# Performance work log

Hardware: AMD Instinct MI355X
Metric: run time of the kernel (lower is better)

## Reference

```python
import jax, jax.numpy as jnp
import numpy as np


def setup_inputs() -> dict:
    key = jax.random.key(0)
    ks = jax.random.split(key, 10)
    N, E, IN, H, OUT = 100000, 1250000, 64, 128, 64
    inp = {
        "x": jax.random.normal(ks[0], (N, IN), dtype=jnp.float32),
        "edge_index": jax.random.randint(ks[1], (2, E), 0, N, dtype=jnp.int64),
        "W1x": jax.random.normal(ks[2], (IN, H), dtype=jnp.float32) * 0.1,
        "b1x": jnp.zeros((H,), jnp.float32),
        "W2x": jax.random.normal(ks[3], (H, H), dtype=jnp.float32) * 0.1,
        "b2x": jnp.zeros((H,), jnp.float32),
        "W1a": jax.random.normal(ks[4], (IN, H), dtype=jnp.float32) * 0.1,
        "b1a": jnp.zeros((H,), jnp.float32),
        "W2a": jax.random.normal(ks[5], (H, H), dtype=jnp.float32) * 0.1,
        "b2a": jnp.zeros((H,), jnp.float32),
        "Wc": jax.random.normal(ks[6], (2 * H, H), dtype=jnp.float32) * 0.1,
        "bc": jnp.zeros((H,), jnp.float32),
        "Wcls": jax.random.normal(ks[7], (H, OUT), dtype=jnp.float32) * 0.1,
        "bcls": jnp.zeros((OUT,), jnp.float32),
        "num_nodes": N,
    }
    return inp


def _normalize_adj(edge_index, num_nodes):
    # add self loops, then D^{-1/2} A D^{-1/2} edge weights (deg counted on rows)
    loops = jnp.arange(num_nodes, dtype=edge_index.dtype)
    ei = jnp.concatenate([edge_index, jnp.stack([loops, loops])], axis=1)
    row, col = ei[0], ei[1]
    deg = jax.ops.segment_sum(jnp.ones(row.shape[0], jnp.float32), row,
                              num_segments=num_nodes)
    dinv = jnp.where(deg > 0, jax.lax.rsqrt(deg), 0.0)
    ew = dinv[row] * dinv[col]
    return row, col, ew


def reference(x, edge_index, W1x, b1x, W2x, b2x, W1a, b1a, W2a, b2a,
              Wc, bc, Wcls, bcls, num_nodes):
    row, col, ew = _normalize_adj(edge_index, num_nodes)
    # sparse adjacency aggregation: gather, scale, scatter-add
    agg = jax.ops.segment_sum(x[col] * ew[:, None], row, num_segments=num_nodes)
    # dual-branch MLPs
    h_x = jax.nn.relu(x @ W1x + b1x) @ W2x + b2x
    h_a = jax.nn.relu(agg @ W1a + b1a) @ W2a + b2a
    h = jnp.concatenate([h_x, h_a], axis=1) @ Wc + bc
    h = jax.nn.relu(h)  # dropout: eval mode (identity)
    return h @ Wcls + bcls
```

## Files before the change

### kernel.cpp

```cpp
#include <hip/hip_runtime.h>
#include <stdint.h>

typedef unsigned short u16;
typedef unsigned int u32;
typedef __attribute__((ext_vector_type(8))) short frag_ab;
typedef __attribute__((ext_vector_type(4))) float f32x4;

__device__ __forceinline__ u16 f2b(float f) {
  unsigned u = __float_as_uint(f);
  return (u16)((u + 0x7fffu + ((u >> 16) & 1u)) >> 16);
}
__device__ __forceinline__ float b2f(u16 u) {
  return __uint_as_float(((unsigned)u) << 16);
}

__device__ __forceinline__ int detect64(const int* __restrict__ ei32) {
  int v = ei32[2 * (threadIdx.x & 63) + 1];
  unsigned long long b = __ballot(v == 0);
  return (b == ~0ULL) ? 1 : 0;
}

__device__ __forceinline__ int edge_at(const void* ei, long pos, int is64) {
  if (is64) return (int)((const long long*)ei)[pos];
  return ((const int*)ei)[pos];
}

__global__ __launch_bounds__(256) void k_bhist_cvt(
    const void* __restrict__ ei, int E, int CH, int NB, int NBpad,
    int* __restrict__ bh,
    const float* __restrict__ x, u16* __restrict__ xb, long n64) {
  __shared__ int cnt[512];
  const int k = blockIdx.x, tid = threadIdx.x;
  const int is64 = detect64((const int*)ei);
  for (long i = ((long)k * 256 + tid) * 8; i < n64; i += 65536L * 8) {
    float4 v0 = *(const float4*)(x + i);
    float4 v1 = *(const float4*)(x + i + 4);
    frag_ab o;
    o[0] = (short)f2b(v0.x); o[1] = (short)f2b(v0.y);
    o[2] = (short)f2b(v0.z); o[3] = (short)f2b(v0.w);
    o[4] = (short)f2b(v1.x); o[5] = (short)f2b(v1.y);
    o[6] = (short)f2b(v1.z); o[7] = (short)f2b(v1.w);
    *(frag_ab*)(xb + i) = o;
  }
  for (int t = tid; t < NB; t += 256) cnt[t] = 0;
  __syncthreads();
  int e0 = k * CH, e1 = min(E, e0 + CH);
  for (int e = e0 + tid; e < e1; e += 256)
    atomicAdd(&cnt[edge_at(ei, e, is64) >> 9], 1);
  __syncthreads();
  for (int t = tid; t < NB; t += 256) bh[k * NBpad + t] = cnt[t];
}

__global__ __launch_bounds__(256) void k_cscan(
    int* __restrict__ bh, int* __restrict__ bstart, int NB, int NBpad, int E) {
  __shared__ int s[256];
  const int b = threadIdx.x;
  int tot = 0;
  if (b < NB)
    for (int k = 0; k < 256; ++k) tot += bh[k * NBpad + b];
  s[b] = (b < NB) ? tot : 0;
  __syncthreads();
  for (int off = 1; off < 256; off <<= 1) {
    int u = (b >= off) ? s[b - off] : 0;
    __syncthreads();
    s[b] += u;
    __syncthreads();
  }
  int excl = s[b] - tot;
  if (b < NB) {
    bstart[b] = excl;
    int run = excl;
    for (int k = 0; k < 256; ++k) {
      int t = bh[k * NBpad + b];
      bh[k * NBpad + b] = run;
      run += t;
    }
  }
  if (b == 0) bstart[NB] = E;
}

__global__ __launch_bounds__(256) void k_partition(
    const void* __restrict__ ei, int E, int CH, int NB, int NBpad,
    const int* __restrict__ bh, u32* __restrict__ staged) {
  __shared__ int cur[512];
  const int k = blockIdx.x, tid = threadIdx.x;
  const int is64 = detect64((const int*)ei);
  for (int t = tid; t < NB; t += 256) cur[t] = bh[k * NBpad + t];
  __syncthreads();
  int e0 = k * CH, e1 = min(E, e0 + CH);
  for (int e = e0 + tid; e < e1; e += 256) {
    int r = edge_at(ei, e, is64);
    int c = edge_at(ei, (long)E + e, is64);
    int pos = atomicAdd(&cur[r >> 9], 1);
    staged[pos] = ((u32)(r & 511) << 23) | (u32)c;
  }
}

__global__ __launch_bounds__(1024) void k_csr_bucket(
    const u32* __restrict__ staged, const int* __restrict__ bstart,
    int* __restrict__ rowptr, float* __restrict__ dinv,
    u32* __restrict__ cols, int N, int E) {
  __shared__ int cnt[512];
  __shared__ int cur[512];
  const int b = blockIdx.x, tid = threadIdx.x;
  const int r0 = b << 9;
  if (tid < 512) cnt[tid] = 0;
  __syncthreads();
  const int j0 = bstart[b], j1 = bstart[b + 1];
  for (int j = j0 + tid; j < j1; j += 1024)
    atomicAdd(&cnt[staged[j] >> 23], 1);
  __syncthreads();
  if (tid < 512) cur[tid] = cnt[tid];
  __syncthreads();
  for (int off = 1; off < 512; off <<= 1) {
    int v = 0;
    if (tid < 512 && tid >= off) v = cur[tid - off];
    __syncthreads();
    if (tid < 512) cur[tid] += v;
    __syncthreads();
  }
  int myStart = 0;
  if (tid < 512) {
    myStart = j0 + cur[tid] - cnt[tid];
    int r = r0 + tid;
    if (r < N) {
      rowptr[r] = myStart;
      dinv[r] = rsqrtf((float)cnt[tid] + 1.0f);
    }
  }
  __syncthreads();
  if (tid < 512) cur[tid] = myStart;
  if (b == 0 && tid == 0) rowptr[N] = E;
  __syncthreads();
  for (int j = j0 + tid; j < j1; j += 1024) {
    u32 v = staged[j];
    int rl = v >> 23;
    int pos = atomicAdd(&cur[rl], 1);
    cols[pos] = v & 0x7FFFFF;
  }
}

__global__ __launch_bounds__(256) void k_aggregate(
    const int* __restrict__ rowptr, const u32* __restrict__ cols,
    const u16* __restrict__ xb, const float* __restrict__ dinv,
    u16* __restrict__ aggb, int N) {
  int q = (blockIdx.x * 256 + threadIdx.x) >> 6;
  int f = threadIdx.x & 63;
  int r0 = q * 2, r1 = q * 2 + 1;
  if (r0 >= N) return;
  const bool has1 = (r1 < N);
  int j0 = rowptr[r0], e0 = rowptr[r0 + 1];
  int j1 = has1 ? rowptr[r1] : 0;
  int e1 = has1 ? rowptr[r1 + 1] : 0;
  float d0 = dinv[r0];
  float d1 = has1 ? dinv[r1] : 0.f;
  float acc0 = b2f(xb[(long)r0 * 64 + f]) * d0;
  float acc1 = has1 ? b2f(xb[(long)r1 * 64 + f]) * d1 : 0.f;
  while (j0 + 4 <= e0 && j1 + 4 <= e1) {
    int ca0 = cols[j0], ca1 = cols[j0 + 1], ca2 = cols[j0 + 2], ca3 = cols[j0 + 3];
    int cb0 = cols[j1], cb1 = cols[j1 + 1], cb2 = cols[j1 + 2], cb3 = cols[j1 + 3];
    float xa0 = b2f(xb[(long)ca0 * 64 + f]);
    float xa1 = b2f(xb[(long)ca1 * 64 + f]);
    float xa2 = b2f(xb[(long)ca2 * 64 + f]);
    float xa3 = b2f(xb[(long)ca3 * 64 + f]);
    float xb0 = b2f(xb[(long)cb0 * 64 + f]);
    float xb1 = b2f(xb[(long)cb1 * 64 + f]);
    float xb2 = b2f(xb[(long)cb2 * 64 + f]);
    float xb3 = b2f(xb[(long)cb3 * 64 + f]);
    float wa0 = dinv[ca0], wa1 = dinv[ca1], wa2 = dinv[ca2], wa3 = dinv[ca3];
    float wb0 = dinv[cb0], wb1 = dinv[cb1], wb2 = dinv[cb2], wb3 = dinv[cb3];
    acc0 = fmaf(xa0, wa0, acc0); acc1 = fmaf(xb0, wb0, acc1);
    acc0 = fmaf(xa1, wa1, acc0); acc1 = fmaf(xb1, wb1, acc1);
    acc0 = fmaf(xa2, wa2, acc0); acc1 = fmaf(xb2, wb2, acc1);
    acc0 = fmaf(xa3, wa3, acc0); acc1 = fmaf(xb3, wb3, acc1);
    j0 += 4; j1 += 4;
  }
  for (; j0 + 4 <= e0; j0 += 4) {
    int c0 = cols[j0], c1 = cols[j0 + 1], c2 = cols[j0 + 2], c3 = cols[j0 + 3];
    float x0 = b2f(xb[(long)c0 * 64 + f]);
    float x1 = b2f(xb[(long)c1 * 64 + f]);
    float x2 = b2f(xb[(long)c2 * 64 + f]);
    float x3 = b2f(xb[(long)c3 * 64 + f]);
    acc0 = fmaf(x0, dinv[c0], acc0);
    acc0 = fmaf(x1, dinv[c1], acc0);
    acc0 = fmaf(x2, dinv[c2], acc0);
    acc0 = fmaf(x3, dinv[c3], acc0);
  }
  for (; j0 < e0; ++j0) {
    int c = cols[j0];
    acc0 = fmaf(b2f(xb[(long)c * 64 + f]), dinv[c], acc0);
  }
  for (; j1 + 4 <= e1; j1 += 4) {
    int c0 = cols[j1], c1 = cols[j1 + 1], c2 = cols[j1 + 2], c3 = cols[j1 + 3];
    float x0 = b2f(xb[(long)c0 * 64 + f]);
    float x1 = b2f(xb[(long)c1 * 64 + f]);
    float x2 = b2f(xb[(long)c2 * 64 + f]);
    float x3 = b2f(xb[(long)c3 * 64 + f]);
    acc1 = fmaf(x0, dinv[c0], acc1);
    acc1 = fmaf(x1, dinv[c1], acc1);
    acc1 = fmaf(x2, dinv[c2], acc1);
    acc1 = fmaf(x3, dinv[c3], acc1);
  }
  for (; j1 < e1; ++j1) {
    int c = cols[j1];
    acc1 = fmaf(b2f(xb[(long)c * 64 + f]), dinv[c], acc1);
  }
  aggb[(long)r0 * 64 + f] = f2b(acc0 * d0);
  if (has1) aggb[(long)r1 * 64 + f] = f2b(acc1 * d1);
}

__global__ __launch_bounds__(256) void k_wpack(
    const float* __restrict__ W1x, const float* __restrict__ W1a,
    const float* __restrict__ W2x, const float* __restrict__ W2a,
    const float* __restrict__ Wc, const float* __restrict__ b2x,
    const float* __restrict__ b2a, const float* __restrict__ bc,
    const float* __restrict__ Wcls,
    u16* __restrict__ W1xf, u16* __restrict__ W1af,
    u16* __restrict__ Wxpf, u16* __restrict__ Wapf,
    u16* __restrict__ Wclsf, float* __restrict__ bp) {
  const int blk = blockIdx.x, t = threadIdx.x;
  if (blk < 128) {
    const bool isX = blk < 64;
    int i = (isX ? blk : blk - 64) * 256 + t;
    const float* W2 = isX ? W2x : W2a;
    const float* wc = isX ? Wc : Wc + 128 * 128;
    int b = i & 7, l = (i >> 3) & 63, fi = i >> 9;
    int kb = fi & 3, nb = fi >> 2;
    int k = kb * 32 + (l >> 4) * 8 + b;
    int n = nb * 16 + (l & 15);
    float s = 0.f;
    for (int m = 0; m < 128; ++m) s = fmaf(W2[k * 128 + m], wc[m * 128 + n], s);
    (isX ? Wxpf : Wapf)[i] = f2b(s);
  } else if (blk < 224) {
    const float* W; u16* dst; int K, Nc, i0;
    if (blk < 160)      { W = W1x;  dst = W1xf;  K = 64;  Nc = 128; i0 = blk - 128; }
    else if (blk < 192) { W = W1a;  dst = W1af;  K = 64;  Nc = 128; i0 = blk - 160; }
    else                { W = Wcls; dst = Wclsf; K = 128; Nc = 64;  i0 = blk - 192; }
    int i = i0 * 256 + t;
    if (i < K * Nc) {
      int b = i & 7, l = (i >> 3) & 63, fi = i >> 9;
      int KB = K >> 5;
      int kb = fi % KB, nb = fi / KB;
      int k = kb * 32 + (l >> 4) * 8 + b;
      int n = nb * 16 + (l & 15);
      dst[i] = f2b(W[k * Nc + n]);
    }
  } else if (t < 128) {
    float s = bc[t];
    for (int m = 0; m < 128; ++m)
      s += b2x[m] * Wc[m * 128 + t] + b2a[m] * Wc[(128 + m) * 128 + t];
    bp[t] = s;
  }
}

__global__ __launch_bounds__(256) void k_mlp(
    const u16* __restrict__ xb, const u16* __restrict__ aggb,
    const u16* __restrict__ W1xf, const u16* __restrict__ W1af,
    const float* __restrict__ b1x, const float* __restrict__ b1a,
    const u16* __restrict__ Wxpf, const u16* __restrict__ Wapf,
    const float* __restrict__ bp,
    const u16* __restrict__ Wclsf, const float* __restrict__ bcls,
    float* __restrict__ out, int N) {
  __shared__ u16 H1[64 * 256];
  __shared__ u16 H2[64 * 128];
  const int w = threadIdx.x >> 6;
  const int lane = threadIdx.x & 63;
  const int m0 = blockIdx.x * 64;
  const int lm = lane & 15;
  const int lq = lane >> 4;

  for (int br = 0; br < 2; ++br) {
    const u16* A = br ? aggb : xb;
    const u16* Wf = br ? W1af : W1xf;
    const float* bias = br ? b1a : b1x;
    frag_ab a[4][2];
#pragma unroll
    for (int rt = 0; rt < 4; ++rt) {
      const u16* ap = A + (long)(m0 + rt * 16 + lm) * 64 + lq * 8;
      a[rt][0] = *(const frag_ab*)(ap);
      a[rt][1] = *(const frag_ab*)(ap + 32);
    }
#pragma unroll
    for (int nbl = 0; nbl < 2; ++nbl) {
      int nb = w * 2 + nbl;
      frag_ab b0 = *(const frag_ab*)(Wf + (size_t)((nb * 2 + 0) * 64 + lane) * 8);
      frag_ab b1 = *(const frag_ab*)(Wf + (size_t)((nb * 2 + 1) * 64 + lane) * 8);
      int col = nb * 16 + lm;
      float bv = bias[col];
#pragma unroll
      for (int rt = 0; rt < 4; ++rt) {
        f32x4 acc = {0.f, 0.f, 0.f, 0.f};
        acc = __builtin_amdgcn_mfma_f32_16x16x32_bf16(a[rt][0], b0, acc, 0, 0, 0);
        acc = __builtin_amdgcn_mfma_f32_16x16x32_bf16(a[rt][1], b1, acc, 0, 0, 0);
#pragma unroll
        for (int r = 0; r < 4; ++r) {
          int row = rt * 16 + lq * 4 + r;
          H1[(row * 256 + br * 128 + col) ^ ((row & 7) << 3)] =
              f2b(fmaxf(acc[r] + bv, 0.f));
        }
      }
    }
  }
  __syncthreads();

#pragma unroll
  for (int nbl = 0; nbl < 2; ++nbl) {
    int nb = w * 2 + nbl;
    f32x4 acc[4] = {{0.f,0.f,0.f,0.f},{0.f,0.f,0.f,0.f},
                    {0.f,0.f,0.f,0.f},{0.f,0.f,0.f,0.f}};
#pragma unroll
    for (int kb = 0; kb < 8; ++kb) {
      const u16* Wf2 = (kb < 4) ? Wxpf : Wapf;
      frag_ab b = *(const frag_ab*)(Wf2 + (size_t)((nb * 4 + (kb & 3)) * 64 + lane) * 8);
#pragma unroll
      for (int rt = 0; rt < 4; ++rt) {
        int row = rt * 16 + lm;
        frag_ab a = *(const frag_ab*)&H1[(row * 256 + kb * 32 + lq * 8) ^ ((lm & 7) << 3)];
        acc[rt] = __builtin_amdgcn_mfma_f32_16x16x32_bf16(a, b, acc[rt], 0, 0, 0);
      }
    }
    int col = nb * 16 + lm;
    float bv = bp[col];
#pragma unroll
    for (int rt = 0; rt < 4; ++rt)
#pragma unroll
      for (int r = 0; r < 4; ++r) {
        int row = rt * 16 + lq * 4 + r;
        H2[(row * 128 + col) ^ ((row & 7) << 3)] = f2b(fmaxf(acc[rt][r] + bv, 0.f));
      }
  }
  __syncthreads();

  {
    const int nb = w;
    f32x4 acc[4] = {{0.f,0.f,0.f,0.f},{0.f,0.f,0.f,0.f},
                    {0.f,0.f,0.f,0.f},{0.f,0.f,0.f,0.f}};
#pragma unroll
    for (int kb = 0; kb < 4; ++kb) {
      frag_ab b = *(const frag_ab*)(Wclsf + (size_t)((nb * 4 + kb) * 64 + lane) * 8);
#pragma unroll
      for (int rt = 0; rt < 4; ++rt) {
        int row = rt * 16 + lm;
        frag_ab a = *(const frag_ab*)&H2[(row * 128 + kb * 32 + lq * 8) ^ ((lm & 7) << 3)];
        acc[rt] = __builtin_amdgcn_mfma_f32_16x16x32_bf16(a, b, acc[rt], 0, 0, 0);
      }
    }
    int col = nb * 16 + lm;
    float bv = bcls[col];
#pragma unroll
    for (int rt = 0; rt < 4; ++rt)
#pragma unroll
      for (int r = 0; r < 4; ++r) {
        int grow = m0 + rt * 16 + lq * 4 + r;
        if (grow < N) out[(long)grow * 64 + col] = acc[rt][r] + bv;
      }
  }
}

extern "C" void kernel_launch(void* const* d_in, const int* in_sizes, int n_in,
                              void* d_out, int out_size, void* d_ws, size_t ws_size,
                              hipStream_t stream) {
  const float* x    = (const float*)d_in[0];
  const void*  ei   = d_in[1];
  const float* W1x  = (const float*)d_in[2];
  const float* b1x  = (const float*)d_in[3];
  const float* W2x  = (const float*)d_in[4];
  const float* b2x  = (const float*)d_in[5];
  const float* W1a  = (const float*)d_in[6];
  const float* b1a  = (const float*)d_in[7];
  const float* W2a  = (const float*)d_in[8];
  const float* b2a  = (const float*)d_in[9];
  const float* Wc   = (const float*)d_in[10];
  const float* bc   = (const float*)d_in[11];
  const float* Wcls = (const float*)d_in[12];
  const float* bcls = (const float*)d_in[13];
  const int N = in_sizes[0] / 64;
  const int E = in_sizes[1] / 2;

  const int NB = (N + 511) >> 9;
  const int NBpad = (NB + 63) & ~63;
  const int CH = (E + 255) / 256;

  float* ws = (float*)d_ws;
  long nAlign = (N + 255) & ~255L;
  float* dinv = ws;
  int*   rowptr = (int*)(ws + nAlign);
  u16*   xb   = (u16*)(ws + 2 * nAlign + 256);
  u16*   aggb = xb + (long)N * 64;
  float* bp   = (float*)(aggb + (long)N * 64);
  u16*   W1xf = (u16*)(bp + 128);
  u16*   W1af = W1xf + 8192;
  u16*   Wxpf = W1af + 8192;
  u16*   Wapf = Wxpf + 16384;
  u16*   Wclsf = Wapf + 16384;
  int*   bh   = (int*)(Wclsf + 8192);
  int*   bstart = bh + 256 * NBpad;
  u32*   staged = (u32*)(bstart + NB + 64);
  u32*   cols   = staged + E;
  float* out = (float*)d_out;

  k_bhist_cvt<<<256, 256, 0, stream>>>(ei, E, CH, NB, NBpad, bh, x, xb, (long)N * 64);
  k_cscan<<<1, 256, 0, stream>>>(bh, bstart, NB, NBpad, E);
  k_partition<<<256, 256, 0, stream>>>(ei, E, CH, NB, NBpad, bh, staged);
  k_csr_bucket<<<NB, 1024, 0, stream>>>(staged, bstart, rowptr, dinv, cols, N, E);
  k_aggregate<<<(N + 7) / 8, 256, 0, stream>>>(rowptr, cols, xb, dinv, aggb, N);
  k_wpack<<<225, 256, 0, stream>>>(W1x, W1a, W2x, W2a, Wc, b2x, b2a, bc, Wcls,
                                   W1xf, W1af, Wxpf, Wapf, Wclsf, bp);
  k_mlp<<<(N + 63) / 64, 256, 0, stream>>>(xb, aggb, W1xf, W1af, b1x, b1a,
                                           Wxpf, Wapf, bp, Wclsf, bcls, out, N);
}
```

Baseline: 159.5 us.

## Fuse neighbor aggregation into MLP kernel via shared-memory AGG tile

Removes the separate aggregation kernel and computes the per-row gathered sum directly inside the MLP kernel, storing it in a swizzled shared-memory tile that feeds the first MFMA layer. This eliminates the global write and re-read of the bf16 aggregate buffer and one kernel launch. The MLP tile is halved from 64 to 32 rows per block so each wave aggregates 8 rows. The trade-off is that weight fragments are reloaded by twice as many blocks, and the irregular gather latency now sits in the same kernel as the MFMA stages, with no overlap between the two phases inside a block.

```diff
diff --git a/kernel.cpp b/kernel.cpp
--- a/kernel.cpp
+++ b/kernel.cpp
@@ -138,75 +138,6 @@
     int pos = atomicAdd(&cur[rl], 1);
     cols[pos] = v & 0x7FFFFF;
   }
-}
-
-__global__ __launch_bounds__(256) void k_aggregate(
-    const int* __restrict__ rowptr, const u32* __restrict__ cols,
-    const u16* __restrict__ xb, const float* __restrict__ dinv,
-    u16* __restrict__ aggb, int N) {
-  int q = (blockIdx.x * 256 + threadIdx.x) >> 6;
-  int f = threadIdx.x & 63;
-  int r0 = q * 2, r1 = q * 2 + 1;
-  if (r0 >= N) return;
-  const bool has1 = (r1 < N);
-  int j0 = rowptr[r0], e0 = rowptr[r0 + 1];
-  int j1 = has1 ? rowptr[r1] : 0;
-  int e1 = has1 ? rowptr[r1 + 1] : 0;
-  float d0 = dinv[r0];
-  float d1 = has1 ? dinv[r1] : 0.f;
-  float acc0 = b2f(xb[(long)r0 * 64 + f]) * d0;
-  float acc1 = has1 ? b2f(xb[(long)r1 * 64 + f]) * d1 : 0.f;
-  while (j0 + 4 <= e0 && j1 + 4 <= e1) {
-    int ca0 = cols[j0], ca1 = cols[j0 + 1], ca2 = cols[j0 + 2], ca3 = cols[j0 + 3];
-    int cb0 = cols[j1], cb1 = cols[j1 + 1], cb2 = cols[j1 + 2], cb3 = cols[j1 + 3];
-    float xa0 = b2f(xb[(long)ca0 * 64 + f]);
-    float xa1 = b2f(xb[(long)ca1 * 64 + f]);
-    float xa2 = b2f(xb[(long)ca2 * 64 + f]);
-    float xa3 = b2f(xb[(long)ca3 * 64 + f]);
-    float xb0 = b2f(xb[(long)cb0 * 64 + f]);
-    float xb1 = b2f(xb[(long)cb1 * 64 + f]);
-    float xb2 = b2f(xb[(long)cb2 * 64 + f]);
-    float xb3 = b2f(xb[(long)cb3 * 64 + f]);
-    float wa0 = dinv[ca0], wa1 = dinv[ca1], wa2 = dinv[ca2], wa3 = dinv[ca3];
-    float wb0 = dinv[cb0], wb1 = dinv[cb1], wb2 = dinv[cb2], wb3 = dinv[cb3];
-    acc0 = fmaf(xa0, wa0, acc0); acc1 = fmaf(xb0, wb0, acc1);
-    acc0 = fmaf(xa1, wa1, acc0); acc1 = fmaf(xb1, wb1, acc1);
-    acc0 = fmaf(xa2, wa2, acc0); acc1 = fmaf(xb2, wb2, acc1);
-    acc0 = fmaf(xa3, wa3, acc0); acc1 = fmaf(xb3, wb3, acc1);
-    j0 += 4; j1 += 4;
-  }
-  for (; j0 + 4 <= e0; j0 += 4) {
-    int c0 = cols[j0], c1 = cols[j0 + 1], c2 = cols[j0 + 2], c3 = cols[j0 + 3];
-    float x0 = b2f(xb[(long)c0 * 64 + f]);
-    float x1 = b2f(xb[(long)c1 * 64 + f]);
-    float x2 = b2f(xb[(long)c2 * 64 + f]);
-    float x3 = b2f(xb[(long)c3 * 64 + f]);
-    acc0 = fmaf(x0, dinv[c0], acc0);
-    acc0 = fmaf(x1, dinv[c1], acc0);
-    acc0 = fmaf(x2, dinv[c2], acc0);
-    acc0 = fmaf(x3, dinv[c3], acc0);
-  }
-  for (; j0 < e0; ++j0) {
-    int c = cols[j0];
-    acc0 = fmaf(b2f(xb[(long)c * 64 + f]), dinv[c], acc0);
-  }
-  for (; j1 + 4 <= e1; j1 += 4) {
-    int c0 = cols[j1], c1 = cols[j1 + 1], c2 = cols[j1 + 2], c3 = cols[j1 + 3];
-    float x0 = b2f(xb[(long)c0 * 64 + f]);
-    float x1 = b2f(xb[(long)c1 * 64 + f]);
-    float x2 = b2f(xb[(long)c2 * 64 + f]);
-    float x3 = b2f(xb[(long)c3 * 64 + f]);
-    acc1 = fmaf(x0, dinv[c0], acc1);
-    acc1 = fmaf(x1, dinv[c1], acc1);
-    acc1 = fmaf(x2, dinv[c2], acc1);
-    acc1 = fmaf(x3, dinv[c3], acc1);
-  }
-  for (; j1 < e1; ++j1) {
-    int c = cols[j1];
-    acc1 = fmaf(b2f(xb[(long)c * 64 + f]), dinv[c], acc1);
-  }
-  aggb[(long)r0 * 64 + f] = f2b(acc0 * d0);
-  if (has1) aggb[(long)r1 * 64 + f] = f2b(acc1 * d1);
 }
 
 __global__ __launch_bounds__(256) void k_wpack(
@@ -253,32 +184,110 @@
   }
 }
 
-__global__ __launch_bounds__(256) void k_mlp(
-    const u16* __restrict__ xb, const u16* __restrict__ aggb,
+__global__ __launch_bounds__(256) void k_fused(
+    const int* __restrict__ rowptr, const u32* __restrict__ cols,
+    const u16* __restrict__ xb, const float* __restrict__ dinv,
     const u16* __restrict__ W1xf, const u16* __restrict__ W1af,
     const float* __restrict__ b1x, const float* __restrict__ b1a,
     const u16* __restrict__ Wxpf, const u16* __restrict__ Wapf,
     const float* __restrict__ bp,
     const u16* __restrict__ Wclsf, const float* __restrict__ bcls,
     float* __restrict__ out, int N) {
-  __shared__ u16 H1[64 * 256];
-  __shared__ u16 H2[64 * 128];
+  __shared__ u16 AGG[32 * 64];
+  __shared__ u16 H1[32 * 256];
+  __shared__ u16 H2[32 * 128];
   const int w = threadIdx.x >> 6;
   const int lane = threadIdx.x & 63;
-  const int m0 = blockIdx.x * 64;
+  const int m0 = blockIdx.x * 32;
   const int lm = lane & 15;
   const int lq = lane >> 4;
+  const int f = lane;
+
+  for (int p = 0; p < 8; p += 2) {
+    const int lr0 = w * 8 + p;
+    const int r0 = m0 + lr0, r1 = r0 + 1;
+    if (r0 >= N) break;
+    const bool has1 = (r1 < N);
+    int j0 = rowptr[r0], e0 = rowptr[r0 + 1];
+    int j1 = has1 ? rowptr[r1] : 0;
+    int e1 = has1 ? rowptr[r1 + 1] : 0;
+    float d0 = dinv[r0];
+    float d1 = has1 ? dinv[r1] : 0.f;
+    float acc0 = b2f(xb[(long)r0 * 64 + f]) * d0;
+    float acc1 = has1 ? b2f(xb[(long)r1 * 64 + f]) * d1 : 0.f;
+    while (j0 + 4 <= e0 && j1 + 4 <= e1) {
+      int ca0 = cols[j0], ca1 = cols[j0 + 1], ca2 = cols[j0 + 2], ca3 = cols[j0 + 3];
+      int cb0 = cols[j1], cb1 = cols[j1 + 1], cb2 = cols[j1 + 2], cb3 = cols[j1 + 3];
+      float xa0 = b2f(xb[(long)ca0 * 64 + f]);
+      float xa1 = b2f(xb[(long)ca1 * 64 + f]);
+      float xa2 = b2f(xb[(long)ca2 * 64 + f]);
+      float xa3 = b2f(xb[(long)ca3 * 64 + f]);
+      float xb0 = b2f(xb[(long)cb0 * 64 + f]);
+      float xb1 = b2f(xb[(long)cb1 * 64 + f]);
+      float xb2 = b2f(xb[(long)cb2 * 64 + f]);
+      float xb3 = b2f(xb[(long)cb3 * 64 + f]);
+      float wa0 = dinv[ca0], wa1 = dinv[ca1], wa2 = dinv[ca2], wa3 = dinv[ca3];
+      float wb0 = dinv[cb0], wb1 = dinv[cb1], wb2 = dinv[cb2], wb3 = dinv[cb3];
+      acc0 = fmaf(xa0, wa0, acc0); acc1 = fmaf(xb0, wb0, acc1);
+      acc0 = fmaf(xa1, wa1, acc0); acc1 = fmaf(xb1, wb1, acc1);
+      acc0 = fmaf(xa2, wa2, acc0); acc1 = fmaf(xb2, wb2, acc1);
+      acc0 = fmaf(xa3, wa3, acc0); acc1 = fmaf(xb3, wb3, acc1);
+      j0 += 4; j1 += 4;
+    }
+    for (; j0 + 4 <= e0; j0 += 4) {
+      int c0 = cols[j0], c1 = cols[j0 + 1], c2 = cols[j0 + 2], c3 = cols[j0 + 3];
+      float x0 = b2f(xb[(long)c0 * 64 + f]);
+      float x1 = b2f(xb[(long)c1 * 64 + f]);
+      float x2 = b2f(xb[(long)c2 * 64 + f]);
+      float x3 = b2f(xb[(long)c3 * 64 + f]);
+      acc0 = fmaf(x0, dinv[c0], acc0);
+      acc0 = fmaf(x1, dinv[c1], acc0);
+      acc0 = fmaf(x2, dinv[c2], acc0);
+      acc0 = fmaf(x3, dinv[c3], acc0);
+    }
+    for (; j0 < e0; ++j0) {
+      int c = cols[j0];
+      acc0 = fmaf(b2f(xb[(long)c * 64 + f]), dinv[c], acc0);
+    }
+    for (; j1 + 4 <= e1; j1 += 4) {
+      int c0 = cols[j1], c1 = cols[j1 + 1], c2 = cols[j1 + 2], c3 = cols[j1 + 3];
+      float x0 = b2f(xb[(long)c0 * 64 + f]);
+      float x1 = b2f(xb[(long)c1 * 64 + f]);
+      float x2 = b2f(xb[(long)c2 * 64 + f]);
+      float x3 = b2f(xb[(long)c3 * 64 + f]);
+      acc1 = fmaf(x0, dinv[c0], acc1);
+      acc1 = fmaf(x1, dinv[c1], acc1);
+      acc1 = fmaf(x2, dinv[c2], acc1);
+      acc1 = fmaf(x3, dinv[c3], acc1);
+    }
+    for (; j1 < e1; ++j1) {
+      int c = cols[j1];
+      acc1 = fmaf(b2f(xb[(long)c * 64 + f]), dinv[c], acc1);
+    }
+    AGG[lr0 * 64 + (f ^ ((lr0 & 7) << 3))] = f2b(acc0 * d0);
+    if (has1) {
+      const int lr1 = lr0 + 1;
+      AGG[lr1 * 64 + (f ^ ((lr1 & 7) << 3))] = f2b(acc1 * d1);
+    }
+  }
+  __syncthreads();
 
   for (int br = 0; br < 2; ++br) {
-    const u16* A = br ? aggb : xb;
     const u16* Wf = br ? W1af : W1xf;
     const float* bias = br ? b1a : b1x;
-    frag_ab a[4][2];
-#pragma unroll
-    for (int rt = 0; rt < 4; ++rt) {
-      const u16* ap = A + (long)(m0 + rt * 16 + lm) * 64 + lq * 8;
-      a[rt][0] = *(const frag_ab*)(ap);
-      a[rt][1] = *(const frag_ab*)(ap + 32);
+    frag_ab a[2][2];
+#pragma unroll
+    for (int rt = 0; rt < 2; ++rt) {
+      if (br == 0) {
+        const u16* ap = xb + (long)(m0 + rt * 16 + lm) * 64 + lq * 8;
+        a[rt][0] = *(const frag_ab*)(ap);
+        a[rt][1] = *(const frag_ab*)(ap + 32);
+      } else {
+        int row = rt * 16 + lm;
+        int key = (lm & 7) << 3;
+        a[rt][0] = *(const frag_ab*)&AGG[row * 64 + ((lq * 8) ^ key)];
+        a[rt][1] = *(const frag_ab*)&AGG[row * 64 + ((32 + lq * 8) ^ key)];
+      }
     }
 #pragma unroll
     for (int nbl = 0; nbl < 2; ++nbl) {
@@ -288,7 +297,7 @@
       int col = nb * 16 + lm;
       float bv = bias[col];
 #pragma unroll
-      for (int rt = 0; rt < 4; ++rt) {
+      for (int rt = 0; rt < 2; ++rt) {
         f32x4 acc = {0.f, 0.f, 0.f, 0.f};
         acc = __builtin_amdgcn_mfma_f32_16x16x32_bf16(a[rt][0], b0, acc, 0, 0, 0);
         acc = __builtin_amdgcn_mfma_f32_16x16x32_bf16(a[rt][1], b1, acc, 0, 0, 0);
@@ -306,14 +315,13 @@
 #pragma unroll
   for (int nbl = 0; nbl < 2; ++nbl) {
     int nb = w * 2 + nbl;
-    f32x4 acc[4] = {{0.f,0.f,0.f,0.f},{0.f,0.f,0.f,0.f},
-                    {0.f,0.f,0.f,0.f},{0.f,0.f,0.f,0.f}};
+    f32x4 acc[2] = {{0.f,0.f,0.f,0.f},{0.f,0.f,0.f,0.f}};
 #pragma unroll
     for (int kb = 0; kb < 8; ++kb) {
       const u16* Wf2 = (kb < 4) ? Wxpf : Wapf;
       frag_ab b = *(const frag_ab*)(Wf2 + (size_t)((nb * 4 + (kb & 3)) * 64 + lane) * 8);
 #pragma unroll
-      for (int rt = 0; rt < 4; ++rt) {
+      for (int rt = 0; rt < 2; ++rt) {
         int row = rt * 16 + lm;
         frag_ab a = *(const frag_ab*)&H1[(row * 256 + kb * 32 + lq * 8) ^ ((lm & 7) << 3)];
         acc[rt] = __builtin_amdgcn_mfma_f32_16x16x32_bf16(a, b, acc[rt], 0, 0, 0);
@@ -322,7 +330,7 @@
     int col = nb * 16 + lm;
     float bv = bp[col];
 #pragma unroll
-    for (int rt = 0; rt < 4; ++rt)
+    for (int rt = 0; rt < 2; ++rt)
 #pragma unroll
       for (int r = 0; r < 4; ++r) {
         int row = rt * 16 + lq * 4 + r;
@@ -333,13 +341,12 @@
 
   {
     const int nb = w;
-    f32x4 acc[4] = {{0.f,0.f,0.f,0.f},{0.f,0.f,0.f,0.f},
-                    {0.f,0.f,0.f,0.f},{0.f,0.f,0.f,0.f}};
+    f32x4 acc[2] = {{0.f,0.f,0.f,0.f},{0.f,0.f,0.f,0.f}};
 #pragma unroll
     for (int kb = 0; kb < 4; ++kb) {
       frag_ab b = *(const frag_ab*)(Wclsf + (size_t)((nb * 4 + kb) * 64 + lane) * 8);
 #pragma unroll
-      for (int rt = 0; rt < 4; ++rt) {
+      for (int rt = 0; rt < 2; ++rt) {
         int row = rt * 16 + lm;
         frag_ab a = *(const frag_ab*)&H2[(row * 128 + kb * 32 + lq * 8) ^ ((lm & 7) << 3)];
         acc[rt] = __builtin_amdgcn_mfma_f32_16x16x32_bf16(a, b, acc[rt], 0, 0, 0);
@@ -348,7 +355,7 @@
     int col = nb * 16 + lm;
     float bv = bcls[col];
 #pragma unroll
-    for (int rt = 0; rt < 4; ++rt)
+    for (int rt = 0; rt < 2; ++rt)
 #pragma unroll
       for (int r = 0; r < 4; ++r) {
         int grow = m0 + rt * 16 + lq * 4 + r;
@@ -386,8 +393,7 @@
   float* dinv = ws;
   int*   rowptr = (int*)(ws + nAlign);
   u16*   xb   = (u16*)(ws + 2 * nAlign + 256);
-  u16*   aggb = xb + (long)N * 64;
-  float* bp   = (float*)(aggb + (long)N * 64);
+  float* bp   = (float*)(xb + (long)N * 64);
   u16*   W1xf = (u16*)(bp + 128);
   u16*   W1af = W1xf + 8192;
   u16*   Wxpf = W1af + 8192;
@@ -403,9 +409,9 @@
   k_cscan<<<1, 256, 0, stream>>>(bh, bstart, NB, NBpad, E);
   k_partition<<<256, 256, 0, stream>>>(ei, E, CH, NB, NBpad, bh, staged);
   k_csr_bucket<<<NB, 1024, 0, stream>>>(staged, bstart, rowptr, dinv, cols, N, E);
-  k_aggregate<<<(N + 7) / 8, 256, 0, stream>>>(rowptr, cols, xb, dinv, aggb, N);
   k_wpack<<<225, 256, 0, stream>>>(W1x, W1a, W2x, W2a, Wc, b2x, b2a, bc, Wcls,
                                    W1xf, W1af, Wxpf, Wapf, Wclsf, bp);
-  k_mlp<<<(N + 63) / 64, 256, 0, stream>>>(xb, aggb, W1xf, W1af, b1x, b1a,
-                                           Wxpf, Wapf, bp, Wclsf, bcls, out, N);
-}
+  k_fused<<<(N + 31) / 32, 256, 0, stream>>>(rowptr, cols, xb, dinv,
+                                             W1xf, W1af, b1x, b1a,
+                                             Wxpf, Wapf, bp, Wclsf, bcls, out, N);
+}
```

Measured after the change: 176.3 us. +10.5%, slower.
